# Performance work log

Measured on AMD Instinct MI355X. Metric: run time of the kernel, lower is better.

Reference implementation:

```python
import jax, jax.numpy as jnp
import numpy as np

B, G, L, S = 4096, 16000, 64, 20000  # batch spots, genes, labels, total spots
LOG_2PI = float(np.log(2.0 * np.pi))


def _log_nb_positive_altparam(x, r, o):
    # NB with total_count r > 0 and logits o (stereoscope parametrization)
    return (jax.lax.lgamma(x + r) - jax.lax.lgamma(r) - jax.lax.lgamma(x + 1.0)
            + x * jax.nn.log_sigmoid(o) + r * jax.nn.log_sigmoid(-o))


def setup_inputs() -> dict:
    key = jax.random.key(0)
    ks = jax.random.split(key, 8)
    x = jax.random.randint(ks[0], (B, G), 0, 100, dtype=jnp.int32)
    y = jax.random.randint(ks[1], (B, 1), 0, L, dtype=jnp.int32)
    ind_x = jax.random.randint(ks[2], (B, 1), 0, S, dtype=jnp.int32)
    W = jax.random.normal(ks[3], (G, L), dtype=jnp.float32)          # fixed dictionary
    px_o = 0.5 * jax.random.normal(ks[4], (G,), dtype=jnp.float32)   # fixed log-odds
    eta = jax.random.normal(ks[5], (G,), dtype=jnp.float32)
    V = jax.random.normal(ks[6], (L + 1, S), dtype=jnp.float32)
    beta = 0.1 * jax.random.normal(ks[7], (G,), dtype=jnp.float32)
    return {"x": x, "y": y, "ind_x": ind_x, "W": W, "px_o": px_o,
            "eta": eta, "V": V, "beta": beta}


def reference(x, y, ind_x, W, px_o, eta, V, beta):
    x_f = x.astype(jnp.float32)                      # [B, G]
    beta_sp = jax.nn.softplus(beta)                  # [G]
    w_sp = jax.nn.softplus(W)                        # [G, L]
    eps_sp = jax.nn.softplus(eta)                    # [G]
    # r_hat = [beta*W | eps]  -> [G, L+1]
    r_hat = jnp.concatenate([beta_sp[:, None] * w_sp, eps_sp[:, None]], axis=1)
    # column-gather from V (embedding lookup over spots), then softplus
    v_ind = jax.nn.softplus(V[:, ind_x[:, 0]])       # [L+1, B]
    # thin matmul, inner dim L+1; px_rate: [B, G]
    px_rate = jnp.einsum("gl,lb->bg", r_hat, v_ind)
    # NB reconstruction loss per spot
    reconst_loss = -jnp.sum(_log_nb_positive_altparam(x_f, px_rate, px_o[None, :]), axis=-1)  # [B]
    # -sum log N(eta; 0, 1)
    neg_log_likelihood_prior = jnp.sum(0.5 * LOG_2PI + 0.5 * eta * eta)
    return (reconst_loss, jnp.float32(0.0), neg_log_likelihood_prior)
```

## Files before the change

kernel.cpp:

```cpp
#include <hip/hip_runtime.h>
#include <hip/hip_bf16.h>
#include <math.h>

#define Gn 16000
#define Bn 4096
#define Ln 64
#define Sn 20000

typedef __attribute__((ext_vector_type(8))) short bf16x8;
typedef __attribute__((ext_vector_type(4))) float f32x4;


__device__ __forceinline__ float softplus_precise(float z) {
    return fmaxf(z, 0.0f) + log1pf(__expf(-fabsf(z)));
}

__device__ __forceinline__ float lgamma_pos8(float z) {
    float p = z * (z + 1.f) * (z + 2.f) * (z + 3.f)
                * (z + 4.f) * (z + 5.f) * (z + 6.f) * (z + 7.f);
    float w = z + 8.f;
    return (w - 0.5f) * __logf(w) - w + 0.9189385332046727f
           + __fdividef(1.0f, 12.0f * w) - __logf(p);
}

__device__ __forceinline__ unsigned short f2bf(float f) {
    union { float f; unsigned int u; } v; v.f = f;
    unsigned int r = v.u + 0x7fff + ((v.u >> 16) & 1);
    return (unsigned short)(r >> 16);
}


__global__ void prep_genes(const float* __restrict__ W,
                           const float* __restrict__ px_o,
                           const float* __restrict__ eta,
                           const float* __restrict__ beta,
                           unsigned short* __restrict__ rhB,
                           float* __restrict__ lsp1,
                           float* __restrict__ lsn,
                           float* __restrict__ eps) {
    int idx = blockIdx.x * 256 + threadIdx.x;
    int g = idx >> 6, l = idx & 63;
    int j = g & 63, gb = g & ~63;
    int c = (j & 3) * 16 + (j >> 2);
    float bsp = softplus_precise(beta[g]);
    rhB[(size_t)(gb + c) * 64 + l] = f2bf(bsp * softplus_precise(W[idx]));
    if (idx < Gn) {
        eps[idx] = softplus_precise(eta[idx]);
        float o = px_o[idx];
        lsp1[idx] = -softplus_precise(-o) - 1.0f;
        lsn[idx]  = -softplus_precise(o);
    }
}

__global__ void prep_spots(const float* __restrict__ V,
                           const int* __restrict__ ind_x,
                           unsigned short* __restrict__ vBg,
                           float* __restrict__ v64) {
    int idx = blockIdx.x * 256 + threadIdx.x;
    int b = idx >> 6, l = idx & 63;
    int s = ind_x[b];
    vBg[idx] = f2bf(softplus_precise(V[l * Sn + s]));
    if (idx < Bn) {
        int s2 = ind_x[idx];
        v64[idx] = softplus_precise(V[Ln * Sn + s2]);
    }
}

__global__ void prior_kernel(const float* __restrict__ eta, float* __restrict__ out) {
    int idx = blockIdx.x * 256 + threadIdx.x;
    float s = 0.f;
    if (idx < Gn) {
        float e = eta[idx];
        s = 0.9189385332046727f + 0.5f * e * e;
    }
    #pragma unroll
    for (int off = 32; off; off >>= 1) s += __shfl_xor(s, off, 64);
    __shared__ float red[4];
    if ((threadIdx.x & 63) == 0) red[threadIdx.x >> 6] = s;
    __syncthreads();
    if (threadIdx.x == 0) atomicAdd(&out[Bn + 1], red[0] + red[1] + red[2] + red[3]);
}


__global__ __launch_bounds__(256) void main_kernel(
    const int*            __restrict__ x,
    const unsigned short* __restrict__ rhB,
    const unsigned short* __restrict__ vBg,
    const float*          __restrict__ v64,
    const float*          __restrict__ lsp1g,
    const float*          __restrict__ lsng,
    const float*          __restrict__ epsg,
    float*                __restrict__ out) {
    __shared__ float lfact[100];

    const int tid = threadIdx.x;
    if (tid < 100) lfact[tid] = lgamma_pos8((float)tid + 1.0f);
    __syncthreads();

    const int g0 = blockIdx.x * 64;
    const int b0 = blockIdx.y * 64;
    const int wave = tid >> 6, lane = tid & 63;
    const int quad = lane >> 4, ln = lane & 15;
    const int mrow  = wave * 16 + ln;
    const int brow0 = b0 + wave * 16 + quad * 4;

    int4 xq[4];
    #pragma unroll
    for (int r = 0; r < 4; r++)
        xq[r] = *(const int4*)(x + (size_t)(brow0 + r) * Gn + g0 + ln * 4);

    const float4 lsp1q = *(const float4*)(lsp1g + g0 + ln * 4);
    const float4 lsnq  = *(const float4*)(lsng  + g0 + ln * 4);
    const float4 epsq  = *(const float4*)(epsg  + g0 + ln * 4);
    const float4 vq    = *(const float4*)(v64 + brow0);

    const unsigned short* aPtr = vBg + (size_t)(b0 + mrow) * 64 + quad * 8;
    bf16x8 af0 = *(const bf16x8*)(aPtr);
    bf16x8 af1 = *(const bf16x8*)(aPtr + 32);

    const unsigned short* bPtr = rhB + (size_t)(g0 + ln) * 64 + quad * 8;
    bf16x8 bf_[4][2];
    #pragma unroll
    for (int nb = 0; nb < 4; nb++) {
        bf_[nb][0] = *(const bf16x8*)(bPtr + nb * 1024);
        bf_[nb][1] = *(const bf16x8*)(bPtr + nb * 1024 + 32);
    }

    f32x4 acc[4];
    #pragma unroll
    for (int nb = 0; nb < 4; nb++) acc[nb] = (f32x4){0.f, 0.f, 0.f, 0.f};
    #pragma unroll
    for (int nb = 0; nb < 4; nb++) {
        acc[nb] = __builtin_amdgcn_mfma_f32_16x16x32_bf16(af0, bf_[nb][0], acc[nb], 0, 0, 0);
        acc[nb] = __builtin_amdgcn_mfma_f32_16x16x32_bf16(af1, bf_[nb][1], acc[nb], 0, 0, 0);
    }

    const float vvr[4]  = {vq.x, vq.y, vq.z, vq.w};
    const float lsp1v[4] = {lsp1q.x, lsp1q.y, lsp1q.z, lsp1q.w};
    const float lsnv[4]  = {lsnq.x, lsnq.y, lsnq.z, lsnq.w};
    const float ev4[4]   = {epsq.x, epsq.y, epsq.z, epsq.w};

    float rowpart[4] = {0.f, 0.f, 0.f, 0.f};
    #pragma unroll
    for (int nb = 0; nb < 4; nb++) {
        #pragma unroll
        for (int r = 0; r < 4; r++) {
            const float rr = fmaf(ev4[nb], vvr[r], acc[nb][r]);
            const int   xi = ((const int*)&xq[r])[nb];
            const float xf = (float)xi;
            const float s  = rr + xf;
            float t = fmaf(s - 0.5f, __logf(s), -lfact[xi]);
            t = fmaf(-(rr - 0.5f), __logf(rr), t);
            t = fmaf(xf, lsp1v[nb], t);
            t = fmaf(rr, lsnv[nb], t);
            rowpart[r] += t;
        }
    }

    #pragma unroll
    for (int r = 0; r < 4; r++) {
        float v = rowpart[r];
        v += __shfl_xor(v, 1, 64);
        v += __shfl_xor(v, 2, 64);
        v += __shfl_xor(v, 4, 64);
        v += __shfl_xor(v, 8, 64);
        if (ln == 0) atomicAdd(&out[brow0 + r], -v);
    }
}


extern "C" void kernel_launch(void* const* d_in, const int* in_sizes, int n_in,
                              void* d_out, int out_size, void* d_ws, size_t ws_size,
                              hipStream_t stream) {
    const int*   x     = (const int*)d_in[0];
    const int*   ind_x = (const int*)d_in[2];
    const float* W     = (const float*)d_in[3];
    const float* px_o  = (const float*)d_in[4];
    const float* eta   = (const float*)d_in[5];
    const float* V     = (const float*)d_in[6];
    const float* beta  = (const float*)d_in[7];
    float* out = (float*)d_out;

    char* wsb = (char*)d_ws;
    unsigned short* rhB  = (unsigned short*)(wsb);
    unsigned short* vBg  = (unsigned short*)(wsb + 2048000);
    float*          v64  = (float*)(wsb + 2572288);
    float*          lsp1 = (float*)(wsb + 2588672);
    float*          lsn  = (float*)(wsb + 2652672);
    float*          eps  = (float*)(wsb + 2716672);

    hipMemsetAsync(d_out, 0, (Bn + 2) * sizeof(float), stream);

    prep_genes<<<(Gn * 64) / 256, 256, 0, stream>>>(W, px_o, eta, beta, rhB, lsp1, lsn, eps);
    prep_spots<<<(Bn * 64) / 256, 256, 0, stream>>>(V, ind_x, vBg, v64);
    prior_kernel<<<(Gn + 255) / 256, 256, 0, stream>>>(eta, out);

    dim3 grid(Gn / 64, Bn / 64);
    main_kernel<<<grid, 256, 0, stream>>>(x, rhB, vBg, v64, lsp1, lsn, eps, out);
}
```

Before: 442.4 us.

## Factor linear rate term out of main loop and switch to log2 arithmetic

The r*log_sigmoid(-o) term is linear in the rate, so its per-spot sum is computed separately as u·softplus(V) with a small gene-reduction kernel and a spot-correction kernel that writes the initial output. The main kernel then drops one load stream and one FMA per element. It also works in base-2 logs with prescaled constants and batches the log evaluations, and it sets a launch-bounds occupancy hint. The price is two extra small launches plus an fp32 reduction order that differs from the original, and the factored term no longer passes through the bf16 matmul.

```diff
diff --git a/kernel.cpp b/kernel.cpp
--- a/kernel.cpp
+++ b/kernel.cpp
@@ -9,6 +9,9 @@
 
 typedef __attribute__((ext_vector_type(8))) short bf16x8;
 typedef __attribute__((ext_vector_type(4))) float f32x4;
+
+#define LN2  0.6931471805599453f
+#define RLN2 1.4426950408889634f
 
 
 __device__ __forceinline__ float softplus_precise(float z) {
@@ -35,8 +38,7 @@
                            const float* __restrict__ eta,
                            const float* __restrict__ beta,
                            unsigned short* __restrict__ rhB,
-                           float* __restrict__ lsp1,
-                           float* __restrict__ lsn,
+                           float* __restrict__ lsp1c,
                            float* __restrict__ eps) {
     int idx = blockIdx.x * 256 + threadIdx.x;
     int g = idx >> 6, l = idx & 63;
@@ -47,8 +49,7 @@
     if (idx < Gn) {
         eps[idx] = softplus_precise(eta[idx]);
         float o = px_o[idx];
-        lsp1[idx] = -softplus_precise(-o) - 1.0f;
-        lsn[idx]  = -softplus_precise(o);
+        lsp1c[idx] = (-softplus_precise(-o) - 1.0f) * RLN2;
     }
 }
 
@@ -66,6 +67,40 @@
     }
 }
 
+__global__ void prep_u(const float* __restrict__ W,
+                       const float* __restrict__ px_o,
+                       const float* __restrict__ eta,
+                       const float* __restrict__ beta,
+                       float* __restrict__ u) {
+    const int l = blockIdx.x;
+    float ss = 0.f;
+    for (int g = threadIdx.x; g < Gn; g += 256) {
+        float lsn = -softplus_precise(px_o[g]);
+        float val = (l == 64) ? softplus_precise(eta[g])
+                              : softplus_precise(beta[g]) * softplus_precise(W[g * 64 + l]);
+        ss += lsn * val;
+    }
+    #pragma unroll
+    for (int off = 32; off; off >>= 1) ss += __shfl_xor(ss, off, 64);
+    __shared__ float red[4];
+    if ((threadIdx.x & 63) == 0) red[threadIdx.x >> 6] = ss;
+    __syncthreads();
+    if (threadIdx.x == 0) u[l] = red[0] + red[1] + red[2] + red[3];
+}
+
+__global__ void spot_corr(const float* __restrict__ V,
+                          const int* __restrict__ ind_x,
+                          const float* __restrict__ u,
+                          float* __restrict__ out) {
+    int b = blockIdx.x * 256 + threadIdx.x;
+    int s = ind_x[b];
+    float c = 0.f;
+    #pragma unroll 5
+    for (int l = 0; l < 65; l++)
+        c = fmaf(u[l], softplus_precise(V[l * Sn + s]), c);
+    out[b] = -c;
+}
+
 __global__ void prior_kernel(const float* __restrict__ eta, float* __restrict__ out) {
     int idx = blockIdx.x * 256 + threadIdx.x;
     float s = 0.f;
@@ -82,19 +117,18 @@
 }
 
 
-__global__ __launch_bounds__(256) void main_kernel(
+__global__ __launch_bounds__(256, 4) void main_kernel(
     const int*            __restrict__ x,
     const unsigned short* __restrict__ rhB,
     const unsigned short* __restrict__ vBg,
     const float*          __restrict__ v64,
-    const float*          __restrict__ lsp1g,
-    const float*          __restrict__ lsng,
+    const float*          __restrict__ lsp1cg,
     const float*          __restrict__ epsg,
     float*                __restrict__ out) {
-    __shared__ float lfact[100];
+    __shared__ float lfact2[100];
 
     const int tid = threadIdx.x;
-    if (tid < 100) lfact[tid] = lgamma_pos8((float)tid + 1.0f);
+    if (tid < 100) lfact2[tid] = lgamma_pos8((float)tid + 1.0f) * RLN2;
     __syncthreads();
 
     const int g0 = blockIdx.x * 64;
@@ -109,9 +143,8 @@
     for (int r = 0; r < 4; r++)
         xq[r] = *(const int4*)(x + (size_t)(brow0 + r) * Gn + g0 + ln * 4);
 
-    const float4 lsp1q = *(const float4*)(lsp1g + g0 + ln * 4);
-    const float4 lsnq  = *(const float4*)(lsng  + g0 + ln * 4);
-    const float4 epsq  = *(const float4*)(epsg  + g0 + ln * 4);
+    const float4 lsp1q = *(const float4*)(lsp1cg + g0 + ln * 4);
+    const float4 epsq  = *(const float4*)(epsg   + g0 + ln * 4);
     const float4 vq    = *(const float4*)(v64 + brow0);
 
     const unsigned short* aPtr = vBg + (size_t)(b0 + mrow) * 64 + quad * 8;
@@ -135,24 +168,35 @@
         acc[nb] = __builtin_amdgcn_mfma_f32_16x16x32_bf16(af1, bf_[nb][1], acc[nb], 0, 0, 0);
     }
 
-    const float vvr[4]  = {vq.x, vq.y, vq.z, vq.w};
+    const float vvr[4]   = {vq.x, vq.y, vq.z, vq.w};
     const float lsp1v[4] = {lsp1q.x, lsp1q.y, lsp1q.z, lsp1q.w};
-    const float lsnv[4]  = {lsnq.x, lsnq.y, lsnq.z, lsnq.w};
     const float ev4[4]   = {epsq.x, epsq.y, epsq.z, epsq.w};
 
     float rowpart[4] = {0.f, 0.f, 0.f, 0.f};
     #pragma unroll
-    for (int nb = 0; nb < 4; nb++) {
+    for (int h = 0; h < 2; h++) {
+        float rr8[8], s8[8];
         #pragma unroll
-        for (int r = 0; r < 4; r++) {
+        for (int jj = 0; jj < 8; jj++) {
+            const int nb = h * 2 + (jj >> 2), r = jj & 3;
             const float rr = fmaf(ev4[nb], vvr[r], acc[nb][r]);
+            rr8[jj] = rr;
+            s8[jj]  = rr + (float)(((const int*)&xq[r])[nb]);
+        }
+        float ls8[8], lr8[8];
+        #pragma unroll
+        for (int jj = 0; jj < 8; jj++) {
+            ls8[jj] = __log2f(s8[jj]);
+            lr8[jj] = __log2f(rr8[jj]);
+        }
+        #pragma unroll
+        for (int jj = 0; jj < 8; jj++) {
+            const int nb = h * 2 + (jj >> 2), r = jj & 3;
             const int   xi = ((const int*)&xq[r])[nb];
             const float xf = (float)xi;
-            const float s  = rr + xf;
-            float t = fmaf(s - 0.5f, __logf(s), -lfact[xi]);
-            t = fmaf(-(rr - 0.5f), __logf(rr), t);
-            t = fmaf(xf, lsp1v[nb], t);
-            t = fmaf(rr, lsnv[nb], t);
+            float t = fmaf(xf, lsp1v[nb], -lfact2[xi]);
+            t = fmaf(0.5f - rr8[jj], lr8[jj], t);
+            t = fmaf(s8[jj] - 0.5f, ls8[jj], t);
             rowpart[r] += t;
         }
     }
@@ -164,7 +208,7 @@
         v += __shfl_xor(v, 2, 64);
         v += __shfl_xor(v, 4, 64);
         v += __shfl_xor(v, 8, 64);
-        if (ln == 0) atomicAdd(&out[brow0 + r], -v);
+        if (ln == 0) atomicAdd(&out[brow0 + r], -LN2 * v);
     }
 }
 
@@ -182,19 +226,21 @@
     float* out = (float*)d_out;
 
     char* wsb = (char*)d_ws;
-    unsigned short* rhB  = (unsigned short*)(wsb);
-    unsigned short* vBg  = (unsigned short*)(wsb + 2048000);
-    float*          v64  = (float*)(wsb + 2572288);
-    float*          lsp1 = (float*)(wsb + 2588672);
-    float*          lsn  = (float*)(wsb + 2652672);
-    float*          eps  = (float*)(wsb + 2716672);
+    unsigned short* rhB   = (unsigned short*)(wsb);
+    unsigned short* vBg   = (unsigned short*)(wsb + 2048000);
+    float*          v64   = (float*)(wsb + 2572288);
+    float*          lsp1c = (float*)(wsb + 2588672);
+    float*          eps   = (float*)(wsb + 2652672);
+    float*          u     = (float*)(wsb + 2716672);
 
     hipMemsetAsync(d_out, 0, (Bn + 2) * sizeof(float), stream);
 
-    prep_genes<<<(Gn * 64) / 256, 256, 0, stream>>>(W, px_o, eta, beta, rhB, lsp1, lsn, eps);
+    prep_genes<<<(Gn * 64) / 256, 256, 0, stream>>>(W, px_o, eta, beta, rhB, lsp1c, eps);
     prep_spots<<<(Bn * 64) / 256, 256, 0, stream>>>(V, ind_x, vBg, v64);
+    prep_u<<<65, 256, 0, stream>>>(W, px_o, eta, beta, u);
+    spot_corr<<<Bn / 256, 256, 0, stream>>>(V, ind_x, u, out);
     prior_kernel<<<(Gn + 255) / 256, 256, 0, stream>>>(eta, out);
 
     dim3 grid(Gn / 64, Bn / 64);
-    main_kernel<<<grid, 256, 0, stream>>>(x, rhB, vBg, v64, lsp1, lsn, eps, out);
-}
+    main_kernel<<<grid, 256, 0, stream>>>(x, rhB, vBg, v64, lsp1c, eps, out);
+}
```

Result: slower. 524.8 us (+18.6%).
